# Performance work log

Measured on AMD Instinct MI355X. Metric: run time of the kernel, lower is better.

## Reference

```python
import jax, jax.numpy as jnp
import numpy as np

N, F, H, T = 100000, 128, 128, 10
E = 1600000
NUM_GRAPHS = 512
BN_EPS = 1e-5


def setup_inputs() -> dict:
    key = jax.random.key(0)
    ks = jax.random.split(key, 16)
    x = jax.random.normal(ks[0], (N, F), dtype=jnp.float32)
    edge_index = jax.random.randint(ks[1], (2, E), 0, N, dtype=jnp.int64)
    batch = jnp.sort(jax.random.randint(ks[2], (N,), 0, NUM_GRAPHS, dtype=jnp.int64))
    s = lambda fin: 1.0 / np.sqrt(fin)
    return {
        "x": x, "edge_index": edge_index, "batch": batch,
        # GINConv 1 MLP: Linear(F,H) -> BN(H) -> ReLU -> Linear(H,H)
        "W1a": jax.random.uniform(ks[3], (F, H), jnp.float32, -s(F), s(F)),
        "b1a": jax.random.uniform(ks[4], (H,), jnp.float32, -s(F), s(F)),
        "g1": jnp.ones((H,), jnp.float32),
        "bt1": jnp.zeros((H,), jnp.float32),
        "W1b": jax.random.uniform(ks[5], (H, H), jnp.float32, -s(H), s(H)),
        "b1b": jax.random.uniform(ks[6], (H,), jnp.float32, -s(H), s(H)),
        # GINConv 2 MLP
        "W2a": jax.random.uniform(ks[7], (H, H), jnp.float32, -s(H), s(H)),
        "b2a": jax.random.uniform(ks[8], (H,), jnp.float32, -s(H), s(H)),
        "g2": jnp.ones((H,), jnp.float32),
        "bt2": jnp.zeros((H,), jnp.float32),
        "W2b": jax.random.uniform(ks[9], (H, H), jnp.float32, -s(H), s(H)),
        "b2b": jax.random.uniform(ks[10], (H,), jnp.float32, -s(H), s(H)),
        # final Linear(H, T)
        "Wl": jax.random.uniform(ks[11], (H, T), jnp.float32, -s(H), s(H)),
        "bl": jax.random.uniform(ks[12], (T,), jnp.float32, -s(H), s(H)),
    }


def _batchnorm(h, gamma, beta):
    # training-mode BN over the node dimension (biased variance), eps=1e-5
    mean = jnp.mean(h, axis=0)
    var = jnp.mean(jnp.square(h - mean), axis=0)
    return (h - mean) * jax.lax.rsqrt(var + BN_EPS) * gamma + beta


def _gin_conv(x, edge_index, Wa, ba, gamma, beta, Wb, bb):
    src, dst = edge_index[0], edge_index[1]
    # sum-aggregate neighbor messages: scatter-add x[src] into dst rows
    agg = jax.ops.segment_sum(x[src], dst, num_segments=x.shape[0])
    h = (x + agg) @ Wa + ba          # eps=0 in GINConv default
    h = jax.nn.relu(_batchnorm(h, gamma, beta))
    return h @ Wb + bb


def reference(x, edge_index, batch, W1a, b1a, g1, bt1, W1b, b1b,
              W2a, b2a, g2, bt2, W2b, b2b, Wl, bl):
    h = jax.nn.relu(_gin_conv(x, edge_index, W1a, b1a, g1, bt1, W1b, b1b))
    h = jax.nn.relu(_gin_conv(h, edge_index, W2a, b2a, g2, bt2, W2b, b2b))
    pooled = jax.ops.segment_sum(h, batch, num_segments=NUM_GRAPHS)  # [G, H]
    return pooled @ Wl + bl  # [G, T]
```

## Files before the change

kernel.cpp:

```cpp
#include <hip/hip_runtime.h>
#include <cstdint>
#include <cstddef>

#define NFEAT 128
#define TGRAPH 10
#define NGRAPHS 512
#define BN_EPS 1e-5f
#define BIN_CHUNK 2048
#define GSPAN 8
#define TSTR 24

typedef __attribute__((ext_vector_type(8))) short bf16x8;
typedef __attribute__((ext_vector_type(4))) float f32x4;
typedef __attribute__((ext_vector_type(2))) float f32x2;

__device__ __forceinline__ float bf2f(short s) {
    union { unsigned u; float f; } c;
    c.u = ((unsigned)(unsigned short)s) << 16;
    return c.f;
}
__device__ __forceinline__ short f2bf(float f) {
    union { float f; unsigned u; } c;
    c.f = f;
    unsigned u = c.u;
    return (short)((u + 0x7fffu + ((u >> 16) & 1u)) >> 16);
}
__device__ __forceinline__ void accp(f32x2& a, unsigned v) {
    union { unsigned u; float f; } lo, hi;
    lo.u = v << 16;
    hi.u = v & 0xffff0000u;
    f32x2 t;
    t[0] = lo.f;
    t[1] = hi.f;
    a += t;
}


__global__ void k_bucket_scan(const int* __restrict__ bhist, int* __restrict__ bbase,
                              int* __restrict__ cur256, int E) {
    __shared__ int s[256];
    int t = threadIdx.x;
    int v = bhist[t];
    s[t] = v;
    __syncthreads();
    for (int off = 1; off < 256; off <<= 1) {
        int x = 0;
        if (t >= off) x = s[t - off];
        __syncthreads();
        if (t >= off) s[t] += x;
        __syncthreads();
    }
    int excl = s[t] - v;
    bbase[t] = excl;
    cur256[t] = excl;
    if (t == 255) bbase[256] = E;
}

__global__ __launch_bounds__(256) void k_bin_scatter(const int* __restrict__ src,
                                                     const int* __restrict__ dst,
                                                     int* __restrict__ cur256,
                                                     int2* __restrict__ binned, int E) {
    __shared__ int hist[256];
    __shared__ int base[256];
    int t = threadIdx.x;
    int e0 = blockIdx.x * BIN_CHUNK;
    int e1 = min(e0 + BIN_CHUNK, E);
    hist[t] = 0;
    __syncthreads();
    for (int e = e0 + t; e < e1; e += 256) {
        int b = dst[e] >> 9;
        atomicAdd(&hist[b], 1);
    }
    __syncthreads();
    int c = hist[t];
    if (c > 0) base[t] = atomicAdd(&cur256[t], c);
    __syncthreads();
    hist[t] = 0;
    __syncthreads();
    for (int e = e0 + t; e < e1; e += 256) {
        int d = dst[e];
        int b = d >> 9;
        int loc = atomicAdd(&hist[b], 1);
        binned[base[b] + loc] = make_int2(src[e], d);
    }
}

__global__ __launch_bounds__(512) void k_bucket_csr(const int2* __restrict__ binned,
                                                    const int* __restrict__ bbase,
                                                    int* __restrict__ rowptr,
                                                    int* __restrict__ adj,
                                                    int N, int E, int nb) {
    __shared__ int deg[512];
    __shared__ int cur[512];
    int b = blockIdx.x;
    int t = threadIdx.x;
    int e0 = bbase[b], e1 = bbase[b + 1];
    deg[t] = 0;
    __syncthreads();
    for (int e = e0 + t; e < e1; e += 512)
        atomicAdd(&deg[binned[e].y & 511], 1);
    __syncthreads();
    int v = deg[t];
    for (int off = 1; off < 512; off <<= 1) {
        int x = 0;
        if (t >= off) x = deg[t - off];
        __syncthreads();
        if (t >= off) deg[t] += x;
        __syncthreads();
    }
    int excl = deg[t] - v;
    cur[t] = excl;
    int node = b * 512 + t;
    if (node < N) rowptr[node] = e0 + excl;
    if (b == nb - 1 && t == 0) rowptr[N] = E;
    __syncthreads();
    for (int e = e0 + t; e < e1; e += 512) {
        int2 p = binned[e];
        int loc = atomicAdd(&cur[p.y & 511], 1);
        adj[e0 + loc] = p.x;
    }
}

__global__ __launch_bounds__(256) void k_prep_hist(const int* __restrict__ dst,
                                                   int* __restrict__ bhist, int E, int hb,
                                                   const float* __restrict__ x,
                                                   short* __restrict__ xbf,
                                                   const float* __restrict__ W0,
                                                   const float* __restrict__ W1,
                                                   const float* __restrict__ W2,
                                                   const float* __restrict__ W3,
                                                   short* __restrict__ Wf, int n4) {
    int t = threadIdx.x;
    if (blockIdx.x < hb) {
        __shared__ int h[256];
        h[t] = 0;
        __syncthreads();
        for (int e = blockIdx.x * 256 + t; e < E; e += hb * 256)
            atomicAdd(&h[dst[e] >> 9], 1);
        __syncthreads();
        if (h[t]) atomicAdd(&bhist[t], h[t]);
        return;
    }
    int i = (blockIdx.x - hb) * 256 + t;
    if (i < n4) {
        float4 v = ((const float4*)x)[i];
        ushort4 o;
        o.x = (unsigned short)f2bf(v.x);
        o.y = (unsigned short)f2bf(v.y);
        o.z = (unsigned short)f2bf(v.z);
        o.w = (unsigned short)f2bf(v.w);
        ((ushort4*)xbf)[i] = o;
    } else {
        int idx = i - n4;
        if (idx < 4 * 16384) {
            int w = idx >> 14, r = idx & 16383;
            int j = r & 7, lane = (r >> 3) & 63, ct = (r >> 9) & 7, kc = r >> 12;
            int k = kc * 32 + (lane >> 4) * 8 + j;
            int n = ct * 16 + (lane & 15);
            const float* W = (w == 0) ? W0 : (w == 1) ? W1 : (w == 2) ? W2 : W3;
            Wf[idx] = f2bf(W[k * NFEAT + n]);
        }
    }
}

__global__ __launch_bounds__(256) void k_agg_gemm(const short* __restrict__ X,
                                                  const int* __restrict__ rowptr,
                                                  const int* __restrict__ adj,
                                                  const short* __restrict__ Wf,
                                                  const float* __restrict__ bias,
                                                  float* __restrict__ stats,
                                                  short* __restrict__ C, int N) {
    __shared__ float s_aux[256];
    __shared__ short c_tile[4][32 * TSTR];
    int tid = threadIdx.x;
    int wave = tid >> 6, lane = tid & 63;
    int quad = lane >> 4, l16 = lane & 15;
    int row_base = blockIdx.x * 128 + wave * 32;

    s_aux[tid] = 0.f;
    __syncthreads();

    const uint4* Xv = (const uint4*)X;

    bf16x8 afrag[2][4];
#pragma unroll
    for (int rt = 0; rt < 2; ++rt) {
        f32x2 acc[4][4];
#pragma unroll
        for (int kc = 0; kc < 4; ++kc)
#pragma unroll
            for (int m = 0; m < 4; ++m) acc[kc][m] = (f32x2){0.f, 0.f};
        int r = row_base + rt * 16 + l16;
        if (r < N) {
            size_t rb = (size_t)r * 16 + quad;
#pragma unroll
            for (int kc = 0; kc < 4; ++kc) {
                uint4 v = Xv[rb + kc * 4];
                accp(acc[kc][0], v.x); accp(acc[kc][1], v.y);
                accp(acc[kc][2], v.z); accp(acc[kc][3], v.w);
            }
            int e = rowptr[r], e1 = rowptr[r + 1];
            for (; e + 2 <= e1; e += 2) {
                size_t n0 = (size_t)adj[e] * 16 + quad;
                size_t n1 = (size_t)adj[e + 1] * 16 + quad;
                uint4 u0[4], u1[4];
#pragma unroll
                for (int kc = 0; kc < 4; ++kc) u0[kc] = Xv[n0 + kc * 4];
#pragma unroll
                for (int kc = 0; kc < 4; ++kc) u1[kc] = Xv[n1 + kc * 4];
#pragma unroll
                for (int kc = 0; kc < 4; ++kc) {
                    accp(acc[kc][0], u0[kc].x); accp(acc[kc][1], u0[kc].y);
                    accp(acc[kc][2], u0[kc].z); accp(acc[kc][3], u0[kc].w);
                    accp(acc[kc][0], u1[kc].x); accp(acc[kc][1], u1[kc].y);
                    accp(acc[kc][2], u1[kc].z); accp(acc[kc][3], u1[kc].w);
                }
            }
            if (e < e1) {
                size_t n0 = (size_t)adj[e] * 16 + quad;
#pragma unroll
                for (int kc = 0; kc < 4; ++kc) {
                    uint4 v = Xv[n0 + kc * 4];
                    accp(acc[kc][0], v.x); accp(acc[kc][1], v.y);
                    accp(acc[kc][2], v.z); accp(acc[kc][3], v.w);
                }
            }
        }
#pragma unroll
        for (int kc = 0; kc < 4; ++kc) {
            bf16x8 f;
#pragma unroll
            for (int m = 0; m < 4; ++m) {
                f[2 * m] = f2bf(acc[kc][m][0]);
                f[2 * m + 1] = f2bf(acc[kc][m][1]);
            }
            afrag[rt][kc] = f;
        }
    }

    f32x4 acc[2][8];
#pragma unroll
    for (int i = 0; i < 2; i++)
#pragma unroll
        for (int j = 0; j < 8; j++) acc[i][j] = (f32x4){0.f, 0.f, 0.f, 0.f};

#pragma unroll
    for (int kc = 0; kc < 4; ++kc) {
        const short* wp = Wf + ((size_t)(kc * 8) * 64 + lane) * 8;
#pragma unroll
        for (int ct = 0; ct < 8; ++ct) {
            bf16x8 b = *(const bf16x8*)(wp + (size_t)ct * 64 * 8);
            acc[0][ct] = __builtin_amdgcn_mfma_f32_16x16x32_bf16(afrag[0][kc], b, acc[0][ct], 0, 0, 0);
            acc[1][ct] = __builtin_amdgcn_mfma_f32_16x16x32_bf16(afrag[1][kc], b, acc[1][ct], 0, 0, 0);
        }
    }

    short* tile = &c_tile[wave][0];
    int row2 = lane >> 1, half = lane & 1;
#pragma unroll
    for (int ct = 0; ct < 8; ++ct) {
        int col = ct * 16 + l16;
        float bv = bias[col];
        float ls = 0.f, ls2 = 0.f;
#pragma unroll
        for (int rt = 0; rt < 2; ++rt) {
#pragma unroll
            for (int reg = 0; reg < 4; ++reg) {
                int lrow = rt * 16 + quad * 4 + reg;
                float v = acc[rt][ct][reg] + bv;
                if (row_base + lrow < N) { ls += v; ls2 += v * v; }
                tile[lrow * TSTR + l16] = f2bf(v);
            }
        }
        ls += __shfl_xor(ls, 16);
        ls += __shfl_xor(ls, 32);
        ls2 += __shfl_xor(ls2, 16);
        ls2 += __shfl_xor(ls2, 32);
        if (quad == 0) {
            atomicAdd(&s_aux[col], ls);
            atomicAdd(&s_aux[NFEAT + col], ls2);
        }
        uint4 val = *(const uint4*)(tile + row2 * TSTR + half * 8);
        int grow = row_base + row2;
        if (grow < N) {
            int col0 = ct * 16 + half * 8;
            size_t addr = ((size_t)(grow >> 4) * 4 + (col0 >> 5)) * 512 +
                          (size_t)((((col0 >> 3) & 3) * 16 + (grow & 15)) * 8);
            *(uint4*)(C + addr) = val;
        }
    }

    __syncthreads();
    if (tid < NFEAT) {
        atomicAdd(&stats[tid], s_aux[tid]);
        atomicAdd(&stats[NFEAT + tid], s_aux[NFEAT + tid]);
    }
}

template <bool BN_RELU_IN, bool RELU_OUT, bool STATS, bool FRAG_OUT, bool POOL>
__global__ __launch_bounds__(256) void k_gemm_mfma(const short* __restrict__ A,
                                                   const short* __restrict__ Wf,
                                                   const float* __restrict__ bias,
                                                   float* __restrict__ stats,
                                                   const float* __restrict__ gamma,
                                                   const float* __restrict__ beta,
                                                   const int* __restrict__ batch,
                                                   float* __restrict__ pooled,
                                                   short* __restrict__ C, int N) {
    __shared__ float s_aux[256];
    __shared__ short c_tile[4][32 * TSTR];
    __shared__ float s_pool[GSPAN][NFEAT];
    int tid = threadIdx.x;
    int wave = tid >> 6, lane = tid & 63;
    int quad = lane >> 4, l16 = lane & 15;
    int row_base = blockIdx.x * 128 + wave * 32;

    int gbase = 0;
    if constexpr (POOL) {
        int first = blockIdx.x * 128;
        gbase = (first < N) ? batch[first] : 0;
        for (int i = tid; i < GSPAN * NFEAT; i += 256) s_pool[i >> 7][i & 127] = 0.f;
    }
    if constexpr (STATS) s_aux[tid] = 0.f;
    if constexpr (BN_RELU_IN) {
        if (tid < NFEAT) {
            float mean = stats[tid] / (float)N;
            float var = stats[NFEAT + tid] / (float)N - mean * mean;
            float inv = rsqrtf(var + BN_EPS);
            float sc = gamma[tid] * inv;
            s_aux[tid] = sc;
            s_aux[NFEAT + tid] = beta[tid] - mean * sc;
        }
    }
    if constexpr (STATS || BN_RELU_IN || POOL) __syncthreads();

    f32x4 acc[2][8];
#pragma unroll
    for (int i = 0; i < 2; i++)
#pragma unroll
        for (int j = 0; j < 8; j++) acc[i][j] = (f32x4){0.f, 0.f, 0.f, 0.f};

    const short* af = A + ((size_t)(blockIdx.x * 8 + wave * 2) * 4) * 512;

#pragma unroll
    for (int kc = 0; kc < 4; ++kc) {
        bf16x8 a0 = *(const bf16x8*)(af + (size_t)kc * 512 + lane * 8);
        bf16x8 a1 = *(const bf16x8*)(af + (size_t)(4 + kc) * 512 + lane * 8);
        if constexpr (BN_RELU_IN) {
            int koff = kc * 32 + quad * 8;
#pragma unroll
            for (int j = 0; j < 8; j++) {
                float sc = s_aux[koff + j];
                float sh = s_aux[NFEAT + koff + j];
                a0[j] = f2bf(fmaxf(bf2f(a0[j]) * sc + sh, 0.f));
                a1[j] = f2bf(fmaxf(bf2f(a1[j]) * sc + sh, 0.f));
            }
        }
        const short* wp = Wf + ((size_t)(kc * 8) * 64 + lane) * 8;
#pragma unroll
        for (int ct = 0; ct < 8; ++ct) {
            bf16x8 b = *(const bf16x8*)(wp + (size_t)ct * 64 * 8);
            acc[0][ct] = __builtin_amdgcn_mfma_f32_16x16x32_bf16(a0, b, acc[0][ct], 0, 0, 0);
            acc[1][ct] = __builtin_amdgcn_mfma_f32_16x16x32_bf16(a1, b, acc[1][ct], 0, 0, 0);
        }
    }

    int dg[8];
    if constexpr (POOL) {
#pragma unroll
        for (int rt = 0; rt < 2; ++rt)
#pragma unroll
            for (int reg = 0; reg < 4; ++reg) {
                int row = row_base + rt * 16 + quad * 4 + reg;
                dg[rt * 4 + reg] = (row < N) ? (batch[row] - gbase) : -1;
            }
    }

    short* tile = &c_tile[wave][0];
    int row2 = lane >> 1, half = lane & 1;
#pragma unroll
    for (int ct = 0; ct < 8; ++ct) {
        int col = ct * 16 + l16;
        float bv = bias[col];
        float ls = 0.f, ls2 = 0.f;
        int cg = -1;
        float ps = 0.f;
#pragma unroll
        for (int rt = 0; rt < 2; ++rt) {
#pragma unroll
            for (int reg = 0; reg < 4; ++reg) {
                int lrow = rt * 16 + quad * 4 + reg;
                float v = acc[rt][ct][reg] + bv;
                if constexpr (RELU_OUT) v = fmaxf(v, 0.f);
                if constexpr (STATS) {
                    if (row_base + lrow < N) { ls += v; ls2 += v * v; }
                }
                if constexpr (POOL) {
                    int d = dg[rt * 4 + reg];
                    if (d != cg) {
                        if (cg >= 0) atomicAdd(&s_pool[cg & (GSPAN - 1)][col], ps);
                        cg = d; ps = 0.f;
                    }
                    if (d >= 0) ps += v;
                } else {
                    tile[lrow * TSTR + l16] = f2bf(v);
                }
            }
        }
        if constexpr (POOL) {
            if (cg >= 0) atomicAdd(&s_pool[cg & (GSPAN - 1)][col], ps);
        }
        if constexpr (STATS) {
            ls += __shfl_xor(ls, 16);
            ls += __shfl_xor(ls, 32);
            ls2 += __shfl_xor(ls2, 16);
            ls2 += __shfl_xor(ls2, 32);
            if (quad == 0) {
                atomicAdd(&s_aux[col], ls);
                atomicAdd(&s_aux[NFEAT + col], ls2);
            }
        }
        if constexpr (!POOL) {
            uint4 val = *(const uint4*)(tile + row2 * TSTR + half * 8);
            int grow = row_base + row2;
            if (grow < N) {
                int col0 = ct * 16 + half * 8;
                if constexpr (FRAG_OUT) {
                    size_t addr = ((size_t)(grow >> 4) * 4 + (col0 >> 5)) * 512 +
                                  (size_t)((((col0 >> 3) & 3) * 16 + (grow & 15)) * 8);
                    *(uint4*)(C + addr) = val;
                } else {
                    *(uint4*)(C + (size_t)grow * NFEAT + col0) = val;
                }
            }
        }
    }

    if constexpr (STATS) {
        __syncthreads();
        if (tid < NFEAT) {
            atomicAdd(&stats[tid], s_aux[tid]);
            atomicAdd(&stats[NFEAT + tid], s_aux[NFEAT + tid]);
        }
    }
    if constexpr (POOL) {
        __syncthreads();
        for (int i = tid; i < GSPAN * NFEAT; i += 256) {
            float v = s_pool[i >> 7][i & 127];
            if (v != 0.f) {
                int gg = gbase + (i >> 7);
                if (gg < NGRAPHS) atomicAdd(&pooled[gg * NFEAT + (i & 127)], v);
            }
        }
    }
}

__global__ void k_final(const float* __restrict__ pooled, const float* __restrict__ Wl,
                        const float* __restrict__ bl, float* __restrict__ out) {
    int idx = blockIdx.x * blockDim.x + threadIdx.x;
    if (idx >= NGRAPHS * TGRAPH) return;
    int g = idx / TGRAPH, t = idx % TGRAPH;
    const float* p = pooled + (size_t)g * NFEAT;
    float acc = bl[t];
#pragma unroll 16
    for (int k = 0; k < NFEAT; ++k) acc += p[k] * Wl[k * TGRAPH + t];
    out[idx] = acc;
}

extern "C" void kernel_launch(void* const* d_in, const int* in_sizes, int n_in,
                              void* d_out, int out_size, void* d_ws, size_t ws_size,
                              hipStream_t stream) {
    const float* x = (const float*)d_in[0];
    const int* ei = (const int*)d_in[1];
    const int* batch = (const int*)d_in[2];
    const float* W1a = (const float*)d_in[3];
    const float* b1a = (const float*)d_in[4];
    const float* g1 = (const float*)d_in[5];
    const float* bt1 = (const float*)d_in[6];
    const float* W1b = (const float*)d_in[7];
    const float* b1b = (const float*)d_in[8];
    const float* W2a = (const float*)d_in[9];
    const float* b2a = (const float*)d_in[10];
    const float* g2 = (const float*)d_in[11];
    const float* bt2 = (const float*)d_in[12];
    const float* W2b = (const float*)d_in[13];
    const float* b2b = (const float*)d_in[14];
    const float* Wl = (const float*)d_in[15];
    const float* bl = (const float*)d_in[16];
    float* out = (float*)d_out;

    int N = in_sizes[2];
    int E = in_sizes[1] / 2;
    int nb = (N + 511) >> 9;
    const int* src = ei;
    const int* dst = ei + E;

    int gemmBlocks = (N + 127) / 128;
    int padRows = gemmBlocks * 128;

    char* ws = (char*)d_ws;
    size_t off = 0;
    auto alloc = [&](size_t bytes) -> void* {
        void* p = ws + off;
        off = (off + bytes + 255) & ~(size_t)255;
        return p;
    };
    short* xbf = (short*)alloc((size_t)N * NFEAT * 2);
    short* ybf = (short*)alloc((size_t)padRows * NFEAT * 2);
    short* hbf = (short*)alloc((size_t)N * NFEAT * 2);
    short* Wf = (short*)alloc((size_t)4 * 16384 * 2);
    int* adj = (int*)alloc((size_t)E * 4);
    int2* binned = (int2*)alloc((size_t)E * 8);
    int* rowptr = (int*)alloc((size_t)(N + 1) * 4);
    int* bbase = (int*)alloc(257 * 4);
    int* cur256 = (int*)alloc(256 * 4);
    int* bhist = (int*)alloc(256 * 4);
    float* stats1 = (float*)alloc(256 * 4);
    float* stats2 = (float*)alloc(256 * 4);
    float* pooled = (float*)alloc((size_t)NGRAPHS * NFEAT * 4);
    size_t zbytes = (char*)(pooled + (size_t)NGRAPHS * NFEAT) - (char*)bhist;

    hipMemsetAsync(bhist, 0, zbytes, stream);

    int n4 = N * NFEAT / 4;
    int prepTot = n4 + 4 * 16384;
    int hb = 784;
    k_prep_hist<<<hb + (prepTot + 255) / 256, 256, 0, stream>>>(
        dst, bhist, E, hb, x, xbf, W1a, W1b, W2a, W2b, Wf, n4);
    k_bucket_scan<<<1, 256, 0, stream>>>(bhist, bbase, cur256, E);
    k_bin_scatter<<<(E + BIN_CHUNK - 1) / BIN_CHUNK, 256, 0, stream>>>(src, dst, cur256, binned, E);
    k_bucket_csr<<<nb, 512, 0, stream>>>(binned, bbase, rowptr, adj, N, E, nb);

    k_agg_gemm<<<gemmBlocks, 256, 0, stream>>>(xbf, rowptr, adj, Wf + 0 * 16384, b1a,
                                               stats1, ybf, N);
    k_gemm_mfma<true, true, false, false, false><<<gemmBlocks, 256, 0, stream>>>(
        ybf, Wf + 1 * 16384, b1b, stats1, g1, bt1, nullptr, nullptr, hbf, N);

    k_agg_gemm<<<gemmBlocks, 256, 0, stream>>>(hbf, rowptr, adj, Wf + 2 * 16384, b2a,
                                               stats2, ybf, N);
    k_gemm_mfma<true, true, false, false, true><<<gemmBlocks, 256, 0, stream>>>(
        ybf, Wf + 3 * 16384, b2b, stats2, g2, bt2, batch, pooled, nullptr, N);

    k_final<<<(NGRAPHS * TGRAPH + 255) / 256, 256, 0, stream>>>(pooled, Wl, bl, out);
}
```

Baseline: 452.4 us.

## Halve rows per wave in aggregation GEMM and prefetch adjacency indices

Each wave in k_agg_gemm now handles 16 rows instead of 32, so the grid has twice as many blocks. The change is meant to raise occupancy and parallelism for the latency-bound neighbor gather, and to cut register pressure by dropping the second row tile. The edge loop now prefetches the next pair of adjacency indices and handles an odd tail with a zero-filled second load. The output tile layout changes to pack two column tiles per store, so global writes are issued every other column tile. In exchange, each W fragment is reused across fewer rows and more blocks issue stats atomics.

Result: no change. 445.3 us (-1.6%).

```diff
diff --git a/kernel.cpp b/kernel.cpp
--- a/kernel.cpp
+++ b/kernel.cpp
@@ -9,6 +9,7 @@
 #define BIN_CHUNK 2048
 #define GSPAN 8
 #define TSTR 24
+#define ATSTR 40
 
 typedef __attribute__((ext_vector_type(8))) short bf16x8;
 typedef __attribute__((ext_vector_type(4))) float f32x4;
@@ -171,78 +172,77 @@
                                                   float* __restrict__ stats,
                                                   short* __restrict__ C, int N) {
     __shared__ float s_aux[256];
-    __shared__ short c_tile[4][32 * TSTR];
+    __shared__ short c_tile[4][16 * ATSTR];
     int tid = threadIdx.x;
     int wave = tid >> 6, lane = tid & 63;
     int quad = lane >> 4, l16 = lane & 15;
-    int row_base = blockIdx.x * 128 + wave * 32;
+    int row_base = blockIdx.x * 64 + wave * 16;
 
     s_aux[tid] = 0.f;
     __syncthreads();
 
     const uint4* Xv = (const uint4*)X;
 
-    bf16x8 afrag[2][4];
-#pragma unroll
-    for (int rt = 0; rt < 2; ++rt) {
-        f32x2 acc[4][4];
-#pragma unroll
-        for (int kc = 0; kc < 4; ++kc)
-#pragma unroll
-            for (int m = 0; m < 4; ++m) acc[kc][m] = (f32x2){0.f, 0.f};
-        int r = row_base + rt * 16 + l16;
-        if (r < N) {
-            size_t rb = (size_t)r * 16 + quad;
+    f32x2 acc[4][4];
+#pragma unroll
+    for (int kc = 0; kc < 4; ++kc)
+#pragma unroll
+        for (int m = 0; m < 4; ++m) acc[kc][m] = (f32x2){0.f, 0.f};
+
+    int r = row_base + l16;
+    if (r < N) {
+        size_t rb = (size_t)r * 16 + quad;
+#pragma unroll
+        for (int kc = 0; kc < 4; ++kc) {
+            uint4 v = Xv[rb + kc * 4];
+            accp(acc[kc][0], v.x); accp(acc[kc][1], v.y);
+            accp(acc[kc][2], v.z); accp(acc[kc][3], v.w);
+        }
+        int e0 = rowptr[r], e1 = rowptr[r + 1];
+        int a0 = (e0 < e1) ? adj[e0] : 0;
+        int a1 = (e0 + 1 < e1) ? adj[e0 + 1] : -1;
+        for (int e = e0; e < e1; e += 2) {
+            int p0 = a0;
+            int p1 = a1;
+            a0 = (e + 2 < e1) ? adj[e + 2] : 0;
+            a1 = (e + 3 < e1) ? adj[e + 3] : -1;
+            size_t n0 = (size_t)p0 * 16 + quad;
+            uint4 u0[4], u1[4];
+#pragma unroll
+            for (int kc = 0; kc < 4; ++kc) u0[kc] = Xv[n0 + kc * 4];
+            if (p1 >= 0) {
+                size_t n1 = (size_t)p1 * 16 + quad;
+#pragma unroll
+                for (int kc = 0; kc < 4; ++kc) u1[kc] = Xv[n1 + kc * 4];
+            } else {
+#pragma unroll
+                for (int kc = 0; kc < 4; ++kc) u1[kc] = make_uint4(0u, 0u, 0u, 0u);
+            }
 #pragma unroll
             for (int kc = 0; kc < 4; ++kc) {
-                uint4 v = Xv[rb + kc * 4];
-                accp(acc[kc][0], v.x); accp(acc[kc][1], v.y);
-                accp(acc[kc][2], v.z); accp(acc[kc][3], v.w);
-            }
-            int e = rowptr[r], e1 = rowptr[r + 1];
-            for (; e + 2 <= e1; e += 2) {
-                size_t n0 = (size_t)adj[e] * 16 + quad;
-                size_t n1 = (size_t)adj[e + 1] * 16 + quad;
-                uint4 u0[4], u1[4];
-#pragma unroll
-                for (int kc = 0; kc < 4; ++kc) u0[kc] = Xv[n0 + kc * 4];
-#pragma unroll
-                for (int kc = 0; kc < 4; ++kc) u1[kc] = Xv[n1 + kc * 4];
-#pragma unroll
-                for (int kc = 0; kc < 4; ++kc) {
-                    accp(acc[kc][0], u0[kc].x); accp(acc[kc][1], u0[kc].y);
-                    accp(acc[kc][2], u0[kc].z); accp(acc[kc][3], u0[kc].w);
-                    accp(acc[kc][0], u1[kc].x); accp(acc[kc][1], u1[kc].y);
-                    accp(acc[kc][2], u1[kc].z); accp(acc[kc][3], u1[kc].w);
-                }
-            }
-            if (e < e1) {
-                size_t n0 = (size_t)adj[e] * 16 + quad;
-#pragma unroll
-                for (int kc = 0; kc < 4; ++kc) {
-                    uint4 v = Xv[n0 + kc * 4];
-                    accp(acc[kc][0], v.x); accp(acc[kc][1], v.y);
-                    accp(acc[kc][2], v.z); accp(acc[kc][3], v.w);
-                }
-            }
-        }
-#pragma unroll
-        for (int kc = 0; kc < 4; ++kc) {
-            bf16x8 f;
-#pragma unroll
-            for (int m = 0; m < 4; ++m) {
-                f[2 * m] = f2bf(acc[kc][m][0]);
-                f[2 * m + 1] = f2bf(acc[kc][m][1]);
-            }
-            afrag[rt][kc] = f;
-        }
-    }
-
-    f32x4 acc[2][8];
-#pragma unroll
-    for (int i = 0; i < 2; i++)
-#pragma unroll
-        for (int j = 0; j < 8; j++) acc[i][j] = (f32x4){0.f, 0.f, 0.f, 0.f};
+                accp(acc[kc][0], u0[kc].x); accp(acc[kc][1], u0[kc].y);
+                accp(acc[kc][2], u0[kc].z); accp(acc[kc][3], u0[kc].w);
+                accp(acc[kc][0], u1[kc].x); accp(acc[kc][1], u1[kc].y);
+                accp(acc[kc][2], u1[kc].z); accp(acc[kc][3], u1[kc].w);
+            }
+        }
+    }
+
+    bf16x8 afrag[4];
+#pragma unroll
+    for (int kc = 0; kc < 4; ++kc) {
+        bf16x8 f;
+#pragma unroll
+        for (int m = 0; m < 4; ++m) {
+            f[2 * m] = f2bf(acc[kc][m][0]);
+            f[2 * m + 1] = f2bf(acc[kc][m][1]);
+        }
+        afrag[kc] = f;
+    }
+
+    f32x4 oacc[8];
+#pragma unroll
+    for (int j = 0; j < 8; j++) oacc[j] = (f32x4){0.f, 0.f, 0.f, 0.f};
 
 #pragma unroll
     for (int kc = 0; kc < 4; ++kc) {
@@ -250,27 +250,23 @@
 #pragma unroll
         for (int ct = 0; ct < 8; ++ct) {
             bf16x8 b = *(const bf16x8*)(wp + (size_t)ct * 64 * 8);
-            acc[0][ct] = __builtin_amdgcn_mfma_f32_16x16x32_bf16(afrag[0][kc], b, acc[0][ct], 0, 0, 0);
-            acc[1][ct] = __builtin_amdgcn_mfma_f32_16x16x32_bf16(afrag[1][kc], b, acc[1][ct], 0, 0, 0);
+            oacc[ct] = __builtin_amdgcn_mfma_f32_16x16x32_bf16(afrag[kc], b, oacc[ct], 0, 0, 0);
         }
     }
 
     short* tile = &c_tile[wave][0];
-    int row2 = lane >> 1, half = lane & 1;
+    int row2 = lane >> 2, q2 = lane & 3;
 #pragma unroll
     for (int ct = 0; ct < 8; ++ct) {
         int col = ct * 16 + l16;
         float bv = bias[col];
         float ls = 0.f, ls2 = 0.f;
 #pragma unroll
-        for (int rt = 0; rt < 2; ++rt) {
-#pragma unroll
-            for (int reg = 0; reg < 4; ++reg) {
-                int lrow = rt * 16 + quad * 4 + reg;
-                float v = acc[rt][ct][reg] + bv;
-                if (row_base + lrow < N) { ls += v; ls2 += v * v; }
-                tile[lrow * TSTR + l16] = f2bf(v);
-            }
+        for (int reg = 0; reg < 4; ++reg) {
+            int lrow = quad * 4 + reg;
+            float v = oacc[ct][reg] + bv;
+            if (row_base + lrow < N) { ls += v; ls2 += v * v; }
+            tile[lrow * ATSTR + (ct & 1) * 16 + l16] = f2bf(v);
         }
         ls += __shfl_xor(ls, 16);
         ls += __shfl_xor(ls, 32);
@@ -280,13 +276,15 @@
             atomicAdd(&s_aux[col], ls);
             atomicAdd(&s_aux[NFEAT + col], ls2);
         }
-        uint4 val = *(const uint4*)(tile + row2 * TSTR + half * 8);
-        int grow = row_base + row2;
-        if (grow < N) {
-            int col0 = ct * 16 + half * 8;
-            size_t addr = ((size_t)(grow >> 4) * 4 + (col0 >> 5)) * 512 +
-                          (size_t)((((col0 >> 3) & 3) * 16 + (grow & 15)) * 8);
-            *(uint4*)(C + addr) = val;
+        if (ct & 1) {
+            uint4 val = *(const uint4*)(tile + row2 * ATSTR + q2 * 8);
+            int grow = row_base + row2;
+            if (grow < N) {
+                int col0 = (ct - 1) * 16 + q2 * 8;
+                size_t addr = ((size_t)(grow >> 4) * 4 + (col0 >> 5)) * 512 +
+                              (size_t)((((col0 >> 3) & 3) * 16 + (grow & 15)) * 8);
+                *(uint4*)(C + addr) = val;
+            }
         }
     }
 
@@ -497,6 +495,7 @@
 
     int gemmBlocks = (N + 127) / 128;
     int padRows = gemmBlocks * 128;
+    int aggBlocks = (N + 63) / 64;
 
     char* ws = (char*)d_ws;
     size_t off = 0;
@@ -531,13 +530,13 @@
     k_bin_scatter<<<(E + BIN_CHUNK - 1) / BIN_CHUNK, 256, 0, stream>>>(src, dst, cur256, binned, E);
     k_bucket_csr<<<nb, 512, 0, stream>>>(binned, bbase, rowptr, adj, N, E, nb);
 
-    k_agg_gemm<<<gemmBlocks, 256, 0, stream>>>(xbf, rowptr, adj, Wf + 0 * 16384, b1a,
-                                               stats1, ybf, N);
+    k_agg_gemm<<<aggBlocks, 256, 0, stream>>>(xbf, rowptr, adj, Wf + 0 * 16384, b1a,
+                                              stats1, ybf, N);
     k_gemm_mfma<true, true, false, false, false><<<gemmBlocks, 256, 0, stream>>>(
         ybf, Wf + 1 * 16384, b1b, stats1, g1, bt1, nullptr, nullptr, hbf, N);
 
-    k_agg_gemm<<<gemmBlocks, 256, 0, stream>>>(hbf, rowptr, adj, Wf + 2 * 16384, b2a,
-                                               stats2, ybf, N);
+    k_agg_gemm<<<aggBlocks, 256, 0, stream>>>(hbf, rowptr, adj, Wf + 2 * 16384, b2a,
+                                              stats2, ybf, N);
     k_gemm_mfma<true, true, false, false, true><<<gemmBlocks, 256, 0, stream>>>(
         ybf, Wf + 3 * 16384, b2b, stats2, g2, bt2, batch, pooled, nullptr, N);
 
```
